# Optimization experiments

Hardware: AMD Instinct MI355X
Metric: run time of the kernel (lower is better)

The kernel has to match this reference:

```python
import jax, jax.numpy as jnp
import numpy as np

FE = 16
L = 32 * FE            # 512 input spatial size
K5 = 5 + 8 * (FE - 1)  # 125, C5 kernel so output is 1x1
F6_OUT = 16 * 24 * FE * FE  # 98304

# LeNet-5 sparse connection table for C3, read off the slicing in ConvC3.forward
C3_GROUPS = [
    [0, 1, 2], [1, 2, 3], [2, 3, 4], [3, 4, 5], [4, 5, 0], [5, 0, 1],
    [0, 1, 2, 3], [1, 2, 3, 4], [2, 3, 4, 5], [3, 4, 5, 0], [4, 5, 0, 1], [5, 0, 1, 2],
    [0, 1, 3, 4], [1, 2, 4, 5], [0, 2, 3, 5], [0, 1, 2, 3, 4, 5],
]

def c3_mask():
    m = np.zeros((16, 6, 1, 1), np.float32)
    for o, g in enumerate(C3_GROUPS):
        m[o, g, 0, 0] = 1.0
    return jnp.asarray(m)

_C3_MASK = c3_mask()

def conv2d(x, w, b):
    # x: (C,H,W) unbatched; w: (O,I,kh,kw); VALID, stride 1
    y = jax.lax.conv_general_dilated(x[None], w, (1, 1), 'VALID',
                                     dimension_numbers=('NCHW', 'OIHW', 'NCHW'))[0]
    return y + b[:, None, None]

def avgpool2(x):
    C, H, W = x.shape
    return x.reshape(C, H // 2, 2, W // 2, 2).mean(axis=(2, 4))

def setup_inputs() -> dict:
    key = jax.random.key(0)
    ks = jax.random.split(key, 6)
    x = jax.random.normal(ks[0], (1, L, L), dtype=jnp.float32)
    W1 = jax.random.normal(ks[1], (6, 1, 5, 5), dtype=jnp.float32) * 0.1
    b1 = jnp.zeros((6,), jnp.float32)
    W3 = jax.random.normal(ks[2], (16, 6, 5, 5), dtype=jnp.float32) * 0.1
    b3 = jnp.zeros((16,), jnp.float32)
    W5 = jax.random.normal(ks[3], (120, 16, K5, K5), dtype=jnp.float32) * 0.01
    b5 = jnp.zeros((120,), jnp.float32)
    W6 = jax.random.normal(ks[4], (F6_OUT, 120), dtype=jnp.float32) * 0.05
    b6 = jnp.zeros((F6_OUT,), jnp.float32)
    W7 = jax.random.normal(ks[5], (54, F6_OUT), dtype=jnp.float32) * 0.01
    b7 = jnp.zeros((54,), jnp.float32)
    return {"x": x, "W1": W1, "b1": b1, "W3": W3, "b3": b3,
            "W5": W5, "b5": b5, "W6": W6, "b6": b6, "W7": W7, "b7": b7}

def reference(x, W1, b1, W3, b3, W5, b5, W6, b6, W7, b7):
    relu = jax.nn.relu
    h = relu(conv2d(x, W1, b1))            # (6, 508, 508)
    h = avgpool2(h)                        # (6, 254, 254)
    # C3: 16 tiny sparse-connected 5x5 convs fused into one masked dense conv
    h = relu(conv2d(h, W3 * _C3_MASK, b3)) # (16, 250, 250)
    h = avgpool2(h)                        # (16, 125, 125)
    h = relu(conv2d(h, W5, b5))            # (120, 1, 1)
    h = h.reshape(-1, 120)                 # (1, 120)
    h = relu(h @ W6.T + b6)                # (1, 98304)
    return h @ W7.T + b7                   # (1, 54)
```

## Files before the change

### kernel.cpp

```cpp
#include <hip/hip_runtime.h>

typedef float f32x4 __attribute__((ext_vector_type(4)));

#define P1 254
#define P2 125
#define C5_K 250000
#define C5_K4 62500
#define C5_CHUNK_F4 5000
#undef C5_CHUNK_F4
#define C5_CHUNK_F4 3125
#define F6_OUT 98304
#define F7_K4 24576
#define F7_CHUNK_F4 2048

#define WS_H2 0
#define WS_H4 400000
#define WS_C5 650000
#define WS_H6 650128

__device__ __forceinline__ float4 nt_load4(const float4* p) {
    f32x4 v = __builtin_nontemporal_load((const f32x4*)p);
    return make_float4(v.x, v.y, v.z, v.w);
}

__global__ __launch_bounds__(256) void c1_s2_kernel(const float* __restrict__ x,
        const float* __restrict__ W1, const float* __restrict__ b1,
        float* __restrict__ h2,
        const float* __restrict__ b5, const float* __restrict__ b7,
        float* __restrict__ c5acc, float* __restrict__ out) {
    if (blockIdx.x == 0) {
        int t = threadIdx.x;
        if (t < 120) c5acc[t] = b5[t];
        if (t >= 128 && t < 182) out[t - 128] = b7[t - 128];
    }
    int t = blockIdx.x * 256 + threadIdx.x;
    const int total = 6 * P1 * P1;
    if (t >= total) return;
    int c  = t / (P1 * P1);
    int r  = t % (P1 * P1);
    int y  = r / P1, x0 = r % P1;

    float w[25];
    #pragma unroll
    for (int k = 0; k < 25; ++k) w[k] = W1[c * 25 + k];

    float p[6][6];
    const float2* xin2 = (const float2*)(x + (2 * y) * 512 + 2 * x0);
    #pragma unroll
    for (int i = 0; i < 6; ++i) {
        float2 a0 = xin2[i * 256 + 0];
        float2 a1 = xin2[i * 256 + 1];
        float2 a2 = xin2[i * 256 + 2];
        p[i][0] = a0.x; p[i][1] = a0.y; p[i][2] = a1.x;
        p[i][3] = a1.y; p[i][4] = a2.x; p[i][5] = a2.y;
    }

    float bias = b1[c];
    float s = 0.f;
    #pragma unroll
    for (int dy = 0; dy < 2; ++dy)
        #pragma unroll
        for (int dx = 0; dx < 2; ++dx) {
            float a = bias;
            #pragma unroll
            for (int kh = 0; kh < 5; ++kh)
                #pragma unroll
                for (int kw = 0; kw < 5; ++kw)
                    a = fmaf(p[dy + kh][dx + kw], w[kh * 5 + kw], a);
            s += fmaxf(a, 0.f);
        }
    h2[t] = 0.25f * s;
}

__global__ __launch_bounds__(256) void c3_s4_kernel(const float* __restrict__ h2,
        const float* __restrict__ W3, const float* __restrict__ b3,
        float* __restrict__ h4) {
    const unsigned char MASK[16] = {7,14,28,56,49,35,15,30,60,57,51,39,27,54,45,63};
    int t = blockIdx.x * 256 + threadIdx.x;
    const int total = 16 * P2 * P2;
    if (t >= total) return;
    int o  = t / (P2 * P2);
    int r  = t % (P2 * P2);
    int y  = r / P2, x0 = r % P2;

    float a00, a01, a10, a11;
    a00 = a01 = a10 = a11 = b3[o];
    unsigned m = MASK[o];

    for (int i = 0; i < 6; ++i) {
        if (!((m >> i) & 1)) continue;
        const float2* hp2 = (const float2*)(h2 + i * P1 * P1 + (2 * y) * P1 + 2 * x0);
        const float* wp = W3 + (o * 6 + i) * 25;
        float w[25];
        #pragma unroll
        for (int k = 0; k < 25; ++k) w[k] = wp[k];
        float p[6][6];
        #pragma unroll
        for (int ii = 0; ii < 6; ++ii) {
            float2 a0 = hp2[ii * 127 + 0];
            float2 a1 = hp2[ii * 127 + 1];
            float2 a2 = hp2[ii * 127 + 2];
            p[ii][0] = a0.x; p[ii][1] = a0.y; p[ii][2] = a1.x;
            p[ii][3] = a1.y; p[ii][4] = a2.x; p[ii][5] = a2.y;
        }
        #pragma unroll
        for (int kh = 0; kh < 5; ++kh)
            #pragma unroll
            for (int kw = 0; kw < 5; ++kw) {
                float wv = w[kh * 5 + kw];
                a00 = fmaf(p[kh][kw],         wv, a00);
                a01 = fmaf(p[kh][kw + 1],     wv, a01);
                a10 = fmaf(p[kh + 1][kw],     wv, a10);
                a11 = fmaf(p[kh + 1][kw + 1], wv, a11);
            }
    }
    h4[t] = 0.25f * (fmaxf(a00, 0.f) + fmaxf(a01, 0.f) + fmaxf(a10, 0.f) + fmaxf(a11, 0.f));
}

__device__ __forceinline__ float block_reduce_256(float v) {
    #pragma unroll
    for (int off = 32; off > 0; off >>= 1) v += __shfl_down(v, off, 64);
    __shared__ float s[4];
    int lane = threadIdx.x & 63, wv = threadIdx.x >> 6;
    if (lane == 0) s[wv] = v;
    __syncthreads();
    return s[0] + s[1] + s[2] + s[3];
}

__global__ __launch_bounds__(256) void c5_kernel(const float* __restrict__ h4,
        const float* __restrict__ W5, float* __restrict__ c5acc) {
    int row = blockIdx.y;
    const float4* wr = (const float4*)(W5 + (size_t)row * C5_K);
    const float4* hv = (const float4*)h4;
    int start = blockIdx.x * C5_CHUNK_F4;
    int end   = start + C5_CHUNK_F4;
    float s = 0.f;
    for (int i = start + (int)threadIdx.x; i < end; i += 256) {
        float4 w = nt_load4(&wr[i]);
        float4 h = hv[i];
        s = fmaf(w.x, h.x, s); s = fmaf(w.y, h.y, s);
        s = fmaf(w.z, h.z, s); s = fmaf(w.w, h.w, s);
    }
    s = block_reduce_256(s);
    if (threadIdx.x == 0) atomicAdd(&c5acc[row], s);
}

#define F6_RPB 128
#define F6_STRIDE 124
__global__ __launch_bounds__(256) void f6_kernel(const float* __restrict__ c5acc,
        const float* __restrict__ W6, const float* __restrict__ b6,
        float* __restrict__ h6) {
    __shared__ float ws6[F6_RPB * F6_STRIDE];
    __shared__ float h5s[120];
    int tid = threadIdx.x;
    int base = blockIdx.x * F6_RPB;
    if (tid < 120) h5s[tid] = fmaxf(c5acc[tid], 0.f);
    const float4* src = (const float4*)(W6 + (size_t)base * 120);
    #pragma unroll
    for (int i = 0; i < 15; ++i) {
        int f4 = tid + i * 256;
        float4 v = nt_load4(&src[f4]);
        int flat = f4 * 4;
        int row = flat / 120;
        int col = flat - row * 120;
        *(float4*)&ws6[row * F6_STRIDE + col] = v;
    }
    __syncthreads();
    int row  = tid >> 1;
    int half = tid & 1;
    const float4* wr4 = (const float4*)&ws6[row * F6_STRIDE + half * 60];
    const float4* hh4 = (const float4*)&h5s[half * 60];
    float a = 0.f;
    #pragma unroll
    for (int j = 0; j < 15; ++j) {
        float4 w = wr4[j], h = hh4[j];
        a = fmaf(w.x, h.x, a); a = fmaf(w.y, h.y, a);
        a = fmaf(w.z, h.z, a); a = fmaf(w.w, h.w, a);
    }
    a += __shfl_xor(a, 1, 64);
    if (half == 0) {
        int o = base + row;
        h6[o] = fmaxf(a + b6[o], 0.f);
    }
}

__global__ __launch_bounds__(256) void f7_kernel(const float* __restrict__ h6,
        const float* __restrict__ W7, float* __restrict__ out) {
    int row = blockIdx.y;
    const float4* wr = (const float4*)(W7 + (size_t)row * (F7_K4 * 4));
    const float4* hv = (const float4*)h6;
    int start = blockIdx.x * F7_CHUNK_F4;
    int end   = start + F7_CHUNK_F4;
    float s = 0.f;
    for (int i = start + (int)threadIdx.x; i < end; i += 256) {
        float4 w = nt_load4(&wr[i]);
        float4 h = hv[i];
        s = fmaf(w.x, h.x, s); s = fmaf(w.y, h.y, s);
        s = fmaf(w.z, h.z, s); s = fmaf(w.w, h.w, s);
    }
    s = block_reduce_256(s);
    if (threadIdx.x == 0) atomicAdd(&out[row], s);
}

extern "C" void kernel_launch(void* const* d_in, const int* in_sizes, int n_in,
                              void* d_out, int out_size, void* d_ws, size_t ws_size,
                              hipStream_t stream) {
    const float* x  = (const float*)d_in[0];
    const float* W1 = (const float*)d_in[1];
    const float* b1 = (const float*)d_in[2];
    const float* W3 = (const float*)d_in[3];
    const float* b3 = (const float*)d_in[4];
    const float* W5 = (const float*)d_in[5];
    const float* b5 = (const float*)d_in[6];
    const float* W6 = (const float*)d_in[7];
    const float* b6 = (const float*)d_in[8];
    const float* W7 = (const float*)d_in[9];
    const float* b7 = (const float*)d_in[10];
    float* out = (float*)d_out;
    float* ws  = (float*)d_ws;

    float* h2 = ws + WS_H2;
    float* h4 = ws + WS_H4;
    float* c5 = ws + WS_C5;
    float* h6 = ws + WS_H6;

    {
        int total = 6 * P1 * P1;
        c1_s2_kernel<<<(total + 255) / 256, 256, 0, stream>>>(x, W1, b1, h2, b5, b7, c5, out);
    }
    {
        int total = 16 * P2 * P2;
        c3_s4_kernel<<<(total + 255) / 256, 256, 0, stream>>>(h2, W3, b3, h4);
    }
    c5_kernel<<<dim3(C5_K4 / C5_CHUNK_F4, 120), 256, 0, stream>>>(h4, W5, c5);
    f6_kernel<<<F6_OUT / F6_RPB, 256, 0, stream>>>(c5, W6, b6, h6);
    f7_kernel<<<dim3(F7_K4 / F7_CHUNK_F4, 54), 256, 0, stream>>>(h6, W7, out);
}
```

Baseline: 273.6 us.

## Fuse F6 and F7 into one kernel and unroll the C5 reduction loop

Merges the F6 and F7 fully connected layers into one kernel. Each block computes 96 F6 outputs into shared memory, then immediately multiplies them against the matching W7 column slice and atomically adds 54 partial sums into the output. This removes one launch and the global round trip of the h6 vector, at the cost of many more atomics on out (1024 blocks × 54) and strided W7 reads of 128 bytes per row. The C5 loop is also fully unrolled with two independent accumulators to raise memory-level parallelism.

```diff
diff --git a/kernel.cpp b/kernel.cpp
--- a/kernel.cpp
+++ b/kernel.cpp
@@ -6,17 +6,17 @@
 #define P2 125
 #define C5_K 250000
 #define C5_K4 62500
-#define C5_CHUNK_F4 5000
-#undef C5_CHUNK_F4
 #define C5_CHUNK_F4 3125
 #define F6_OUT 98304
-#define F7_K4 24576
-#define F7_CHUNK_F4 2048
+
+#define F6_RPB 96
+#define F6_STRIDE 124
+#define F6_NBLK (F6_OUT / F6_RPB)
+#define F6_PANEL_F4 (F6_RPB * 120 / 4)
 
 #define WS_H2 0
 #define WS_H4 400000
 #define WS_C5 650000
-#define WS_H6 650128
 
 __device__ __forceinline__ float4 nt_load4(const float4* p) {
     f32x4 v = __builtin_nontemporal_load((const f32x4*)p);
@@ -132,74 +132,86 @@
     int row = blockIdx.y;
     const float4* wr = (const float4*)(W5 + (size_t)row * C5_K);
     const float4* hv = (const float4*)h4;
-    int start = blockIdx.x * C5_CHUNK_F4;
-    int end   = start + C5_CHUNK_F4;
-    float s = 0.f;
-    for (int i = start + (int)threadIdx.x; i < end; i += 256) {
+    int i = blockIdx.x * C5_CHUNK_F4 + (int)threadIdx.x;
+    float s0 = 0.f, s1 = 0.f;
+    #pragma unroll
+    for (int k = 0; k < 6; ++k) {
+        float4 wa = nt_load4(&wr[i]);
+        float4 wb = nt_load4(&wr[i + 256]);
+        float4 ha = hv[i];
+        float4 hb = hv[i + 256];
+        s0 = fmaf(wa.x, ha.x, s0); s0 = fmaf(wa.y, ha.y, s0);
+        s0 = fmaf(wa.z, ha.z, s0); s0 = fmaf(wa.w, ha.w, s0);
+        s1 = fmaf(wb.x, hb.x, s1); s1 = fmaf(wb.y, hb.y, s1);
+        s1 = fmaf(wb.z, hb.z, s1); s1 = fmaf(wb.w, hb.w, s1);
+        i += 512;
+    }
+    if (threadIdx.x < 53) {
         float4 w = nt_load4(&wr[i]);
         float4 h = hv[i];
-        s = fmaf(w.x, h.x, s); s = fmaf(w.y, h.y, s);
-        s = fmaf(w.z, h.z, s); s = fmaf(w.w, h.w, s);
-    }
-    s = block_reduce_256(s);
+        s0 = fmaf(w.x, h.x, s0); s0 = fmaf(w.y, h.y, s0);
+        s0 = fmaf(w.z, h.z, s0); s0 = fmaf(w.w, h.w, s0);
+    }
+    float s = block_reduce_256(s0 + s1);
     if (threadIdx.x == 0) atomicAdd(&c5acc[row], s);
 }
 
-#define F6_RPB 128
-#define F6_STRIDE 124
-__global__ __launch_bounds__(256) void f6_kernel(const float* __restrict__ c5acc,
+__global__ __launch_bounds__(256) void f6f7_kernel(const float* __restrict__ c5acc,
         const float* __restrict__ W6, const float* __restrict__ b6,
-        float* __restrict__ h6) {
+        const float* __restrict__ W7, float* __restrict__ out) {
     __shared__ float ws6[F6_RPB * F6_STRIDE];
     __shared__ float h5s[120];
+    __shared__ float h6s[F6_RPB];
+    __shared__ float part[3 * 54];
     int tid = threadIdx.x;
     int base = blockIdx.x * F6_RPB;
     if (tid < 120) h5s[tid] = fmaxf(c5acc[tid], 0.f);
     const float4* src = (const float4*)(W6 + (size_t)base * 120);
     #pragma unroll
-    for (int i = 0; i < 15; ++i) {
-        int f4 = tid + i * 256;
-        float4 v = nt_load4(&src[f4]);
-        int flat = f4 * 4;
-        int row = flat / 120;
-        int col = flat - row * 120;
-        *(float4*)&ws6[row * F6_STRIDE + col] = v;
-    }
-    __syncthreads();
-    int row  = tid >> 1;
-    int half = tid & 1;
-    const float4* wr4 = (const float4*)&ws6[row * F6_STRIDE + half * 60];
-    const float4* hh4 = (const float4*)&h5s[half * 60];
-    float a = 0.f;
-    #pragma unroll
-    for (int j = 0; j < 15; ++j) {
-        float4 w = wr4[j], h = hh4[j];
-        a = fmaf(w.x, h.x, a); a = fmaf(w.y, h.y, a);
-        a = fmaf(w.z, h.z, a); a = fmaf(w.w, h.w, a);
-    }
-    a += __shfl_xor(a, 1, 64);
-    if (half == 0) {
-        int o = base + row;
-        h6[o] = fmaxf(a + b6[o], 0.f);
-    }
-}
-
-__global__ __launch_bounds__(256) void f7_kernel(const float* __restrict__ h6,
-        const float* __restrict__ W7, float* __restrict__ out) {
-    int row = blockIdx.y;
-    const float4* wr = (const float4*)(W7 + (size_t)row * (F7_K4 * 4));
-    const float4* hv = (const float4*)h6;
-    int start = blockIdx.x * F7_CHUNK_F4;
-    int end   = start + F7_CHUNK_F4;
-    float s = 0.f;
-    for (int i = start + (int)threadIdx.x; i < end; i += 256) {
-        float4 w = nt_load4(&wr[i]);
-        float4 h = hv[i];
-        s = fmaf(w.x, h.x, s); s = fmaf(w.y, h.y, s);
-        s = fmaf(w.z, h.z, s); s = fmaf(w.w, h.w, s);
-    }
-    s = block_reduce_256(s);
-    if (threadIdx.x == 0) atomicAdd(&out[row], s);
+    for (int it = 0; it < 12; ++it) {
+        int f4 = tid + it * 256;
+        if (f4 < F6_PANEL_F4) {
+            float4 v = nt_load4(&src[f4]);
+            int flat = f4 * 4;
+            int row = flat / 120;
+            int col = flat - row * 120;
+            *(float4*)&ws6[row * F6_STRIDE + col] = v;
+        }
+    }
+    __syncthreads();
+    if (tid < 2 * F6_RPB) {
+        int row  = tid >> 1;
+        int half = tid & 1;
+        const float4* wr4 = (const float4*)&ws6[row * F6_STRIDE + half * 60];
+        const float4* hh4 = (const float4*)&h5s[half * 60];
+        float a = 0.f;
+        #pragma unroll
+        for (int j = 0; j < 15; ++j) {
+            float4 w = wr4[j], h = hh4[j];
+            a = fmaf(w.x, h.x, a); a = fmaf(w.y, h.y, a);
+            a = fmaf(w.z, h.z, a); a = fmaf(w.w, h.w, a);
+        }
+        a += __shfl_xor(a, 1, 64);
+        if (half == 0) h6s[row] = fmaxf(a + b6[base + row], 0.f);
+    }
+    __syncthreads();
+    if (tid < 162) {
+        int j = tid % 54, seg = tid / 54;
+        const float4* w7 = (const float4*)(W7 + (size_t)j * F6_OUT + base + seg * 32);
+        const float* hh = &h6s[seg * 32];
+        float p = 0.f;
+        #pragma unroll
+        for (int q = 0; q < 8; ++q) {
+            float4 w = nt_load4(&w7[q]);
+            p = fmaf(w.x, hh[4 * q + 0], p); p = fmaf(w.y, hh[4 * q + 1], p);
+            p = fmaf(w.z, hh[4 * q + 2], p); p = fmaf(w.w, hh[4 * q + 3], p);
+        }
+        part[tid] = p;
+    }
+    __syncthreads();
+    if (tid < 54) {
+        atomicAdd(&out[tid], part[tid] + part[54 + tid] + part[108 + tid]);
+    }
 }
 
 extern "C" void kernel_launch(void* const* d_in, const int* in_sizes, int n_in,
@@ -222,7 +234,6 @@
     float* h2 = ws + WS_H2;
     float* h4 = ws + WS_H4;
     float* c5 = ws + WS_C5;
-    float* h6 = ws + WS_H6;
 
     {
         int total = 6 * P1 * P1;
@@ -233,6 +244,5 @@
         c3_s4_kernel<<<(total + 255) / 256, 256, 0, stream>>>(h2, W3, b3, h4);
     }
     c5_kernel<<<dim3(C5_K4 / C5_CHUNK_F4, 120), 256, 0, stream>>>(h4, W5, c5);
-    f6_kernel<<<F6_OUT / F6_RPB, 256, 0, stream>>>(c5, W6, b6, h6);
-    f7_kernel<<<dim3(F7_K4 / F7_CHUNK_F4, 54), 256, 0, stream>>>(h6, W7, out);
-}
+    f6f7_kernel<<<F6_NBLK, 256, 0, stream>>>(c5, W6, b6, W7, out);
+}
```

Result: slower. 283.1 us (+3.5%).
